# Kernel optimization log

Hardware: AMD Instinct MI355X
Metric: run time of the kernel (lower is better)

## Reference

```python
import jax, jax.numpy as jnp
import numpy as np

M, K, D = 4, 2048, 32
N, C, H, W = 8, M * D, 64, 64


def setup_inputs() -> dict:
    key = jax.random.key(0)
    k1, k2 = jax.random.split(key)
    latent = jax.random.normal(k1, (N, C, H, W), dtype=jnp.float32)
    codebook = jax.random.normal(k2, (M, K, D), dtype=jnp.float32)
    return {"latent": latent, "codebook": codebook}


def reference(latent, codebook):
    n, c, h, w = latent.shape
    m, k, d = codebook.shape
    # [n,C,h,w] -> [n,h,w,m,d]
    q = jnp.transpose(latent, (0, 2, 3, 1)).reshape(n, h, w, m, d)
    q2 = jnp.sum(q * q, axis=-1, keepdims=True)          # [n,h,w,m,1]
    c2 = jnp.sum(codebook * codebook, axis=-1)           # [m,k]
    inter = jnp.einsum('nhwmd,mkd->nhwmk', q, codebook)  # [n,h,w,m,k]
    distance = -(q2 + c2 - 2.0 * inter)
    return jnp.argmax(distance, axis=-1)                 # [n,h,w,m] int
```

## Files before the change

### kernel.cpp

```cpp
#include <hip/hip_runtime.h>

#define M_ 4
#define K_ 2048
#define D_ 32
#define HW_ 4096
#define NHW_ 32768
#define NT 128

#define CBH_OFF 0
#define CBL_OFF (M_*K_*D_*2)
#define H_OFF   (CBL_OFF*2)
#define K1_OFF  (H_OFF + M_*K_*4)
#define K2_OFF  (K1_OFF + M_*NHW_*4)

typedef __attribute__((ext_vector_type(8))) short bf16x8;
typedef __attribute__((ext_vector_type(4))) float f32x4;

__device__ __forceinline__ short bf16_rte(float x, float* back) {
    unsigned u = __float_as_uint(x);
    unsigned r = (u + 0x7FFFu + ((u >> 16) & 1u)) >> 16;
    *back = __uint_as_float(r << 16);
    return (short)(r & 0xFFFFu);
}

__global__ __launch_bounds__(256) void prep_kernel(const float* __restrict__ cb,
                                                   unsigned char* __restrict__ ws) {
    int t = blockIdx.x * 256 + threadIdx.x;
    const float* src = cb + (size_t)t * D_;
    short* dh = (short*)(ws + CBH_OFF) + (size_t)t * D_;
    short* dl = (short*)(ws + CBL_OFF) + (size_t)t * D_;
    float* hp = (float*)(ws + H_OFF);
    bf16x8 vh[4], vl[4];
    float c2 = 0.f;
    #pragma unroll
    for (int d = 0; d < D_; ++d) {
        float x = src[d];
        float hf, lf;
        short hb = bf16_rte(x, &hf);
        short lb = bf16_rte(x - hf, &lf);
        vh[d >> 3][d & 7] = hb;
        vl[d >> 3][d & 7] = lb;
        c2 = fmaf(x, x, c2);
    }
    #pragma unroll
    for (int i = 0; i < 4; ++i) {
        *(bf16x8*)(dh + i * 8) = vh[i];
        *(bf16x8*)(dl + i * 8) = vl[i];
    }
    hp[t] = 0.5f * c2;
}

__global__ __launch_bounds__(256) void score_kernel(const float* __restrict__ latent,
        const unsigned char* __restrict__ ws,
        int* __restrict__ k1o, int* __restrict__ k2o) {
    __shared__ float s_h[M_ * K_];
    const int tid = threadIdx.x;
    {
        const float4* src = (const float4*)(ws + H_OFF);
        float4* dst = (float4*)s_h;
        #pragma unroll
        for (int i = 0; i < 8; ++i) dst[tid + i * 256] = src[tid + i * 256];
    }
    __syncthreads();

    const int m    = tid >> 6;
    const int L    = tid & 63;
    const int col  = L & 15;
    const int krow = L >> 4;
    const int posbase = blockIdx.x * 64;
    const int n   = posbase >> 12;
    const int hwb = posbase & (HW_ - 1);

    bf16x8 qh[4], ql[4];
    const float* lp = latent + ((size_t)n * (M_ * D_) + m * D_) * HW_ + hwb;
    #pragma unroll
    for (int g = 0; g < 4; ++g) {
        #pragma unroll
        for (int j = 0; j < 8; ++j) {
            float x = lp[(size_t)(krow * 8 + j) * HW_ + g * 16 + col];
            float hf, lf;
            short hb = bf16_rte(x, &hf);
            short lb = bf16_rte(x - hf, &lf);
            qh[g][j] = hb;
            ql[g][j] = lb;
        }
    }

    const short* ah = (const short*)(ws + CBH_OFF) + ((size_t)m * K_ + col) * D_ + krow * 8;
    const short* al = (const short*)(ws + CBL_OFF) + ((size_t)m * K_ + col) * D_ + krow * 8;

    float b1[4], b2[4]; int k1[4], k2[4];
    #pragma unroll
    for (int g = 0; g < 4; ++g) { b1[g] = b2[g] = -3.402823466e+38f; k1[g] = k2[g] = 0; }

    int kb = krow * 4;

    #pragma unroll 2
    for (int t = 0; t < NT; ++t) {
        bf16x8 ch = *(const bf16x8*)(ah + (size_t)t * (16 * D_));
        bf16x8 cl = *(const bf16x8*)(al + (size_t)t * (16 * D_));
        f32x4 mh = *(const f32x4*)&s_h[m * K_ + t * 16 + krow * 4];
        f32x4 c0;
        c0[0] = -mh[0]; c0[1] = -mh[1]; c0[2] = -mh[2]; c0[3] = -mh[3];
        #pragma unroll
        for (int g = 0; g < 4; ++g) {
            f32x4 a = __builtin_amdgcn_mfma_f32_16x16x32_bf16(cl, qh[g], c0, 0, 0, 0);
            a = __builtin_amdgcn_mfma_f32_16x16x32_bf16(ch, ql[g], a, 0, 0, 0);
            a = __builtin_amdgcn_mfma_f32_16x16x32_bf16(ch, qh[g], a, 0, 0, 0);
            #pragma unroll
            for (int r = 0; r < 4; ++r) {
                float s = a[r];
                int kr = kb + r;
                bool gt = s > b1[g];
                float ss = gt ? b1[g] : s;
                int   sk = gt ? k1[g] : kr;
                b1[g] = gt ? s  : b1[g];
                k1[g] = gt ? kr : k1[g];
                bool g2 = ss > b2[g];
                b2[g] = g2 ? ss : b2[g];
                k2[g] = g2 ? sk : k2[g];
            }
        }
        kb += 16;
    }

    #pragma unroll
    for (int g = 0; g < 4; ++g) {
        #pragma unroll
        for (int off = 16; off <= 32; off <<= 1) {
            float ob1 = __shfl_xor(b1[g], off);
            int   ok1 = __shfl_xor(k1[g], off);
            float ob2 = __shfl_xor(b2[g], off);
            int   ok2 = __shfl_xor(k2[g], off);
            bool awin = (b1[g] > ob1) || (b1[g] == ob1 && k1[g] < ok1);
            float ts = awin ? b1[g] : ob1;  int tk = awin ? k1[g] : ok1;
            float ls = awin ? ob1 : b1[g];  int lk = awin ? ok1 : k1[g];
            float ms = awin ? b2[g] : ob2;  int mk = awin ? k2[g] : ok2;
            bool lwin = (ls > ms) || (ls == ms && lk < mk);
            b1[g] = ts; k1[g] = tk;
            b2[g] = lwin ? ls : ms;
            k2[g] = lwin ? lk : mk;
        }
        if (L < 16) {
            int pos = posbase + g * 16 + L;
            k1o[m * NHW_ + pos] = k1[g];
            k2o[m * NHW_ + pos] = k2[g];
        }
    }
}

__device__ __forceinline__ float score_fp32(const float* __restrict__ q,
                                            const float4* __restrict__ c) {
    float d0 = 0, d1 = 0, d2 = 0, d3 = 0, e0 = 0, e1 = 0, e2 = 0, e3 = 0;
    #pragma unroll
    for (int v = 0; v < 8; ++v) {
        float4 cv = c[v];
        d0 = fmaf(q[v * 4 + 0], cv.x, d0);
        d1 = fmaf(q[v * 4 + 1], cv.y, d1);
        d2 = fmaf(q[v * 4 + 2], cv.z, d2);
        d3 = fmaf(q[v * 4 + 3], cv.w, d3);
        e0 = fmaf(cv.x, cv.x, e0);
        e1 = fmaf(cv.y, cv.y, e1);
        e2 = fmaf(cv.z, cv.z, e2);
        e3 = fmaf(cv.w, cv.w, e3);
    }
    return ((d0 + d1) + (d2 + d3)) - 0.5f * ((e0 + e1) + (e2 + e3));
}

__global__ __launch_bounds__(256) void rescore_kernel(const float* __restrict__ latent,
        const float* __restrict__ cb, const unsigned char* __restrict__ ws,
        int* __restrict__ out) {
    int t = blockIdx.x * 256 + threadIdx.x;
    int m = t >> 15;
    int pos = t & (NHW_ - 1);
    int n = pos >> 12;
    int hw = pos & (HW_ - 1);
    const int* k1a = (const int*)(ws + K1_OFF);
    const int* k2a = (const int*)(ws + K2_OFF);
    int k1 = k1a[t], k2 = k2a[t];
    const float* lp = latent + ((size_t)n * (M_ * D_) + m * D_) * HW_ + hw;
    float q[D_];
    #pragma unroll
    for (int d = 0; d < D_; ++d) q[d] = lp[(size_t)d * HW_];
    float s1 = score_fp32(q, (const float4*)(cb + ((size_t)m * K_ + k1) * D_));
    float s2 = score_fp32(q, (const float4*)(cb + ((size_t)m * K_ + k2) * D_));
    int win = (s2 > s1 || (s2 == s1 && k2 < k1)) ? k2 : k1;
    out[(size_t)pos * M_ + m] = win;
}

extern "C" void kernel_launch(void* const* d_in, const int* in_sizes, int n_in,
                              void* d_out, int out_size, void* d_ws, size_t ws_size,
                              hipStream_t stream) {
    const float* latent   = (const float*)d_in[0];
    const float* codebook = (const float*)d_in[1];
    unsigned char* ws = (unsigned char*)d_ws;
    int* out = (int*)d_out;
    prep_kernel<<<(M_ * K_) / 256, 256, 0, stream>>>(codebook, ws);
    score_kernel<<<NHW_ / 64, 256, 0, stream>>>(latent, ws,
                                                (int*)(ws + K1_OFF), (int*)(ws + K2_OFF));
    rescore_kernel<<<(NHW_ * M_) / 256, 256, 0, stream>>>(latent, codebook, ws, out);
}
```

Measured before the change: 115.2 us.

## Fuse scoring and rescoring with split-K waves and margin-based exact fallback

Merges the score and rescore kernels into one launch. The 2048-entry codebook is split across two waves per subcodebook, the per-candidate top-2 bookkeeping becomes a fmed3-based second-best value, and the full-precision check runs in-kernel on only the top candidate. If the fp32 score of that candidate fails to beat the runner-up bound by EPS, the wave falls back to an exact brute-force fp32 search. This removes the intermediate k1/k2 workspace traffic, one launch, the LDS copy of the norms, and one fp32 rescore per position. In exchange it adds a data-dependent slow path that is serialized across each wave.

```diff
diff --git a/kernel.cpp b/kernel.cpp
--- a/kernel.cpp
+++ b/kernel.cpp
@@ -5,13 +5,12 @@
 #define D_ 32
 #define HW_ 4096
 #define NHW_ 32768
-#define NT 128
-
-#define CBH_OFF 0
-#define CBL_OFF (M_*K_*D_*2)
-#define H_OFF   (CBL_OFF*2)
-#define K1_OFF  (H_OFF + M_*K_*4)
-#define K2_OFF  (K1_OFF + M_*NHW_*4)
+
+#define EPS 0.01f
+
+#define CH_OFF 0
+#define CL_OFF (M_*K_*D_*2)
+#define HN_OFF (CL_OFF*2)
 
 typedef __attribute__((ext_vector_type(8))) short bf16x8;
 typedef __attribute__((ext_vector_type(4))) float f32x4;
@@ -27,9 +26,9 @@
                                                    unsigned char* __restrict__ ws) {
     int t = blockIdx.x * 256 + threadIdx.x;
     const float* src = cb + (size_t)t * D_;
-    short* dh = (short*)(ws + CBH_OFF) + (size_t)t * D_;
-    short* dl = (short*)(ws + CBL_OFF) + (size_t)t * D_;
-    float* hp = (float*)(ws + H_OFF);
+    short* dh = (short*)(ws + CH_OFF) + (size_t)t * D_;
+    short* dl = (short*)(ws + CL_OFF) + (size_t)t * D_;
+    float* hn = (float*)(ws + HN_OFF);
     bf16x8 vh[4], vl[4];
     float c2 = 0.f;
     #pragma unroll
@@ -47,106 +46,7 @@
         *(bf16x8*)(dh + i * 8) = vh[i];
         *(bf16x8*)(dl + i * 8) = vl[i];
     }
-    hp[t] = 0.5f * c2;
-}
-
-__global__ __launch_bounds__(256) void score_kernel(const float* __restrict__ latent,
-        const unsigned char* __restrict__ ws,
-        int* __restrict__ k1o, int* __restrict__ k2o) {
-    __shared__ float s_h[M_ * K_];
-    const int tid = threadIdx.x;
-    {
-        const float4* src = (const float4*)(ws + H_OFF);
-        float4* dst = (float4*)s_h;
-        #pragma unroll
-        for (int i = 0; i < 8; ++i) dst[tid + i * 256] = src[tid + i * 256];
-    }
-    __syncthreads();
-
-    const int m    = tid >> 6;
-    const int L    = tid & 63;
-    const int col  = L & 15;
-    const int krow = L >> 4;
-    const int posbase = blockIdx.x * 64;
-    const int n   = posbase >> 12;
-    const int hwb = posbase & (HW_ - 1);
-
-    bf16x8 qh[4], ql[4];
-    const float* lp = latent + ((size_t)n * (M_ * D_) + m * D_) * HW_ + hwb;
-    #pragma unroll
-    for (int g = 0; g < 4; ++g) {
-        #pragma unroll
-        for (int j = 0; j < 8; ++j) {
-            float x = lp[(size_t)(krow * 8 + j) * HW_ + g * 16 + col];
-            float hf, lf;
-            short hb = bf16_rte(x, &hf);
-            short lb = bf16_rte(x - hf, &lf);
-            qh[g][j] = hb;
-            ql[g][j] = lb;
-        }
-    }
-
-    const short* ah = (const short*)(ws + CBH_OFF) + ((size_t)m * K_ + col) * D_ + krow * 8;
-    const short* al = (const short*)(ws + CBL_OFF) + ((size_t)m * K_ + col) * D_ + krow * 8;
-
-    float b1[4], b2[4]; int k1[4], k2[4];
-    #pragma unroll
-    for (int g = 0; g < 4; ++g) { b1[g] = b2[g] = -3.402823466e+38f; k1[g] = k2[g] = 0; }
-
-    int kb = krow * 4;
-
-    #pragma unroll 2
-    for (int t = 0; t < NT; ++t) {
-        bf16x8 ch = *(const bf16x8*)(ah + (size_t)t * (16 * D_));
-        bf16x8 cl = *(const bf16x8*)(al + (size_t)t * (16 * D_));
-        f32x4 mh = *(const f32x4*)&s_h[m * K_ + t * 16 + krow * 4];
-        f32x4 c0;
-        c0[0] = -mh[0]; c0[1] = -mh[1]; c0[2] = -mh[2]; c0[3] = -mh[3];
-        #pragma unroll
-        for (int g = 0; g < 4; ++g) {
-            f32x4 a = __builtin_amdgcn_mfma_f32_16x16x32_bf16(cl, qh[g], c0, 0, 0, 0);
-            a = __builtin_amdgcn_mfma_f32_16x16x32_bf16(ch, ql[g], a, 0, 0, 0);
-            a = __builtin_amdgcn_mfma_f32_16x16x32_bf16(ch, qh[g], a, 0, 0, 0);
-            #pragma unroll
-            for (int r = 0; r < 4; ++r) {
-                float s = a[r];
-                int kr = kb + r;
-                bool gt = s > b1[g];
-                float ss = gt ? b1[g] : s;
-                int   sk = gt ? k1[g] : kr;
-                b1[g] = gt ? s  : b1[g];
-                k1[g] = gt ? kr : k1[g];
-                bool g2 = ss > b2[g];
-                b2[g] = g2 ? ss : b2[g];
-                k2[g] = g2 ? sk : k2[g];
-            }
-        }
-        kb += 16;
-    }
-
-    #pragma unroll
-    for (int g = 0; g < 4; ++g) {
-        #pragma unroll
-        for (int off = 16; off <= 32; off <<= 1) {
-            float ob1 = __shfl_xor(b1[g], off);
-            int   ok1 = __shfl_xor(k1[g], off);
-            float ob2 = __shfl_xor(b2[g], off);
-            int   ok2 = __shfl_xor(k2[g], off);
-            bool awin = (b1[g] > ob1) || (b1[g] == ob1 && k1[g] < ok1);
-            float ts = awin ? b1[g] : ob1;  int tk = awin ? k1[g] : ok1;
-            float ls = awin ? ob1 : b1[g];  int lk = awin ? ok1 : k1[g];
-            float ms = awin ? b2[g] : ob2;  int mk = awin ? k2[g] : ok2;
-            bool lwin = (ls > ms) || (ls == ms && lk < mk);
-            b1[g] = ts; k1[g] = tk;
-            b2[g] = lwin ? ls : ms;
-            k2[g] = lwin ? lk : mk;
-        }
-        if (L < 16) {
-            int pos = posbase + g * 16 + L;
-            k1o[m * NHW_ + pos] = k1[g];
-            k2o[m * NHW_ + pos] = k2[g];
-        }
-    }
+    hn[t] = -0.5f * c2;
 }
 
 __device__ __forceinline__ float score_fp32(const float* __restrict__ q,
@@ -167,25 +67,143 @@
     return ((d0 + d1) + (d2 + d3)) - 0.5f * ((e0 + e1) + (e2 + e3));
 }
 
-__global__ __launch_bounds__(256) void rescore_kernel(const float* __restrict__ latent,
-        const float* __restrict__ cb, const unsigned char* __restrict__ ws,
+__global__ __launch_bounds__(512) void score_kernel(
+        const float* __restrict__ latent,
+        const float* __restrict__ codebook,
+        const unsigned char* __restrict__ ws,
         int* __restrict__ out) {
-    int t = blockIdx.x * 256 + threadIdx.x;
-    int m = t >> 15;
-    int pos = t & (NHW_ - 1);
-    int n = pos >> 12;
-    int hw = pos & (HW_ - 1);
-    const int* k1a = (const int*)(ws + K1_OFF);
-    const int* k2a = (const int*)(ws + K2_OFF);
-    int k1 = k1a[t], k2 = k2a[t];
-    const float* lp = latent + ((size_t)n * (M_ * D_) + m * D_) * HW_ + hw;
-    float q[D_];
-    #pragma unroll
-    for (int d = 0; d < D_; ++d) q[d] = lp[(size_t)d * HW_];
-    float s1 = score_fp32(q, (const float4*)(cb + ((size_t)m * K_ + k1) * D_));
-    float s2 = score_fp32(q, (const float4*)(cb + ((size_t)m * K_ + k2) * D_));
-    int win = (s2 > s1 || (s2 == s1 && k2 < k1)) ? k2 : k1;
-    out[(size_t)pos * M_ + m] = win;
+    __shared__ float s_b1[2][M_][64];
+    __shared__ int   s_k1[2][M_][64];
+    __shared__ float s_b2[2][M_][64];
+
+    const int tid  = threadIdx.x;
+    const int wave = tid >> 6;
+    const int L    = tid & 63;
+    const int m    = wave & 3;
+    const int kh   = wave >> 2;
+    const int col  = L & 15;
+    const int krow = L >> 4;
+    const int posbase = blockIdx.x * 64;
+    const int n   = posbase >> 12;
+    const int hwb = posbase & (HW_ - 1);
+
+    bf16x8 qh[4], ql[4];
+    const float* lp = latent + ((size_t)n * (M_ * D_) + m * D_) * HW_ + hwb;
+    #pragma unroll
+    for (int g = 0; g < 4; ++g)
+        #pragma unroll
+        for (int j = 0; j < 8; ++j) {
+            float x = lp[(size_t)(krow * 8 + j) * HW_ + g * 16 + col];
+            float hf, lf;
+            qh[g][j] = bf16_rte(x, &hf);
+            ql[g][j] = bf16_rte(x - hf, &lf);
+        }
+
+    const short* ah = (const short*)(ws + CH_OFF)
+                      + ((size_t)m * K_ + kh * 1024 + col) * D_ + krow * 8;
+    const short* al = (const short*)(ws + CL_OFF)
+                      + ((size_t)m * K_ + kh * 1024 + col) * D_ + krow * 8;
+    const float* hn = (const float*)(ws + HN_OFF) + m * K_ + kh * 1024 + krow * 4;
+
+    float b1[4], b2[4];
+    int   k1[4];
+    #pragma unroll
+    for (int g = 0; g < 4; ++g) { b1[g] = b2[g] = -3.402823466e+38f; k1[g] = 0; }
+
+    const int kbase = kh * 1024 + krow * 4;
+
+    for (int t = 0; t < 64; ++t) {
+        bf16x8 ch = *(const bf16x8*)(ah + (size_t)t * (16 * D_));
+        bf16x8 cl = *(const bf16x8*)(al + (size_t)t * (16 * D_));
+        f32x4  c0 = *(const f32x4*)(hn + t * 16);
+        const int kt = kbase + t * 16;
+        #pragma unroll
+        for (int g = 0; g < 4; ++g) {
+            f32x4 a = __builtin_amdgcn_mfma_f32_16x16x32_bf16(cl, qh[g], c0, 0, 0, 0);
+            a = __builtin_amdgcn_mfma_f32_16x16x32_bf16(ch, ql[g], a, 0, 0, 0);
+            a = __builtin_amdgcn_mfma_f32_16x16x32_bf16(ch, qh[g], a, 0, 0, 0);
+            #pragma unroll
+            for (int r = 0; r < 4; ++r) {
+                float s = a[r];
+                b2[g] = __builtin_amdgcn_fmed3f(b1[g], b2[g], s);
+                bool gt = s > b1[g];
+                k1[g] = gt ? (kt + r) : k1[g];
+                b1[g] = gt ? s : b1[g];
+            }
+        }
+    }
+
+    #pragma unroll
+    for (int g = 0; g < 4; ++g) {
+        #pragma unroll
+        for (int off = 16; off <= 32; off <<= 1) {
+            float ob1 = __shfl_xor(b1[g], off);
+            int   ok1 = __shfl_xor(k1[g], off);
+            float ob2 = __shfl_xor(b2[g], off);
+            float mn  = fminf(b1[g], ob1);
+            b2[g] = fmaxf(mn, fmaxf(b2[g], ob2));
+            bool awin = (b1[g] > ob1) || (b1[g] == ob1 && k1[g] < ok1);
+            b1[g] = awin ? b1[g] : ob1;
+            k1[g] = awin ? k1[g] : ok1;
+        }
+    }
+    if (L < 16) {
+        #pragma unroll
+        for (int g = 0; g < 4; ++g) {
+            s_b1[kh][m][g * 16 + L] = b1[g];
+            s_k1[kh][m][g * 16 + L] = k1[g];
+            s_b2[kh][m][g * 16 + L] = b2[g];
+        }
+    }
+    __syncthreads();
+
+    if (wave < 4) {
+        const int pl = tid >> 2;
+        const int mm = tid & 3;
+        const int pos = posbase + pl;
+
+        float A1 = s_b1[0][mm][pl]; int I1 = s_k1[0][mm][pl]; float A2 = s_b2[0][mm][pl];
+        float B1 = s_b1[1][mm][pl]; int J1 = s_k1[1][mm][pl]; float B2 = s_b2[1][mm][pl];
+        float b2m = fmaxf(fminf(A1, B1), fmaxf(A2, B2));
+        bool awin = (A1 > B1) || (A1 == B1 && I1 < J1);
+        int K1 = awin ? I1 : J1;
+
+        const float* lq = latent + ((size_t)n * (M_ * D_) + mm * D_) * HW_ + (hwb + pl);
+        float q[D_];
+        #pragma unroll
+        for (int d = 0; d < D_; ++d) q[d] = lq[(size_t)d * HW_];
+        float sx = score_fp32(q, (const float4*)(codebook + ((size_t)mm * K_ + K1) * D_));
+        bool conf = (sx > b2m + EPS);
+        int result = K1;
+
+        unsigned long long need = __ballot(!conf);
+        while (need) {
+            int bI = __ffsll((unsigned long long)need) - 1;
+            need &= need - 1;
+            int pl_b = wave * 16 + (bI >> 2);
+            int mm_b = bI & 3;
+            const float* lqb = latent + ((size_t)n * (M_ * D_) + mm_b * D_) * HW_ + (hwb + pl_b);
+            float qq[D_];
+            #pragma unroll
+            for (int d = 0; d < D_; ++d) qq[d] = lqb[(size_t)d * HW_];
+            float bs = -3.402823466e+38f;
+            int   bk = 0;
+            for (int i = 0; i < 32; ++i) {
+                int k = L + 64 * i;
+                float s = score_fp32(qq, (const float4*)(codebook + ((size_t)mm_b * K_ + k) * D_));
+                if (s > bs || (s == bs && k < bk)) { bs = s; bk = k; }
+            }
+            #pragma unroll
+            for (int off = 1; off <= 32; off <<= 1) {
+                float os = __shfl_xor(bs, off);
+                int   ok = __shfl_xor(bk, off);
+                if (os > bs || (os == bs && ok < bk)) { bs = os; bk = ok; }
+            }
+            if (L == bI) result = bk;
+        }
+
+        out[(size_t)pos * M_ + mm] = result;
+    }
 }
 
 extern "C" void kernel_launch(void* const* d_in, const int* in_sizes, int n_in,
@@ -196,7 +214,5 @@
     unsigned char* ws = (unsigned char*)d_ws;
     int* out = (int*)d_out;
     prep_kernel<<<(M_ * K_) / 256, 256, 0, stream>>>(codebook, ws);
-    score_kernel<<<NHW_ / 64, 256, 0, stream>>>(latent, ws,
-                                                (int*)(ws + K1_OFF), (int*)(ws + K2_OFF));
-    rescore_kernel<<<(NHW_ * M_) / 256, 256, 0, stream>>>(latent, codebook, ws, out);
-}
+    score_kernel<<<NHW_ / 64, 512, 0, stream>>>(latent, codebook, ws, out);
+}
```

Result: slower. 151.1 us (+31.1%).
